# Kernel optimization log

Hardware: AMD Instinct MI355X
Metric: run time of the kernel (lower is better)

Reference implementation:

```python
import jax, jax.numpy as jnp
import numpy as np

# ragged segment lengths (sum = 100000), 16 graphs of varying size
LENGTHS = np.array([3000, 5000, 7000, 2000, 9000, 4000, 6000, 8000,
                    1000, 10000, 5500, 6500, 7500, 4500, 9500, 11500], dtype=np.int64)

B, N, C_IN, K_DIM, Q_DIM, C_OUT = 4, 100000, 256, 64, 64, 128


def setup_inputs() -> dict:
    key = jax.random.key(0)
    ks = jax.random.split(key, 6)
    features = jax.random.normal(ks[0], (B, N, C_IN), dtype=jnp.float32)
    # linear-layer params (stored as [in, out]; torch Linear computes x @ W.T + b)
    Wk = jax.random.normal(ks[1], (C_IN, K_DIM), dtype=jnp.float32) / np.sqrt(C_IN)
    bk = jnp.zeros((K_DIM,), dtype=jnp.float32)
    Wq = jax.random.normal(ks[2], (C_IN, Q_DIM), dtype=jnp.float32) / np.sqrt(C_IN)
    bq = jnp.zeros((Q_DIM,), dtype=jnp.float32)
    Wv = jax.random.normal(ks[3], (C_IN, C_OUT), dtype=jnp.float32) / np.sqrt(C_IN)
    return {"features": features, "lengths": LENGTHS,
            "Wk": Wk, "bk": bk, "Wq": Wq, "bq": bq, "Wv": Wv}


def reference(features, lengths, Wk, bk, Wq, bq, Wv):
    # projections + (elu + 1) feature map for keys/queries
    k = jax.nn.elu(features @ Wk + bk) + 1.0   # [B, N, K]
    q = jax.nn.elu(features @ Wq + bq) + 1.0   # [B, N, Q]
    v = features @ Wv                           # [B, N, O]
    # static ragged offsets (lengths is a concrete numpy array)
    offs = np.concatenate([[0], np.cumsum(np.asarray(lengths))]).astype(np.int64)
    outs = []
    for i in range(len(offs) - 1):  # loop over fixed small set of graphs
        s, e = int(offs[i]), int(offs[i + 1])
        ktv = jnp.einsum('bnk,bno->bko', k[:, s:e], v[:, s:e])   # per-segment K^T V
        outs.append(jnp.einsum('bnq,bqo->bno', q[:, s:e], ktv))  # Q (K^T V)
    return jnp.concatenate(outs, axis=1)  # [B, N, O]
```

## Files before the change

### kernel.cpp

```cpp
#include <hip/hip_runtime.h>

#define B_ 4
#define N_ 100000

typedef unsigned short u16;
typedef unsigned int u32;
typedef __attribute__((ext_vector_type(8))) __bf16 bf16x8;
typedef __attribute__((ext_vector_type(4))) float floatx4;

__device__ const int d_OFFS[17]  = {0,3000,8000,15000,17000,26000,30000,36000,44000,45000,55000,60500,67000,74500,79000,88500,100000};
__device__ const int d_CH128[17] = {0,24,64,119,135,206,238,285,348,356,435,478,529,588,624,699,789};

__device__ __forceinline__ u16 f2bf(float f) {
    union { float f; unsigned u; } x; x.f = f;
    unsigned r = x.u + 0x7fffu + ((x.u >> 16) & 1u);
    return (u16)(r >> 16);
}

union U4 { u32 u[4]; bf16x8 v; uint4 q; };

__global__ void prep_kernel(const float* __restrict__ Wk, const float* __restrict__ bk,
                            const float* __restrict__ Wq, const float* __restrict__ bq,
                            const float* __restrict__ Wv,
                            u16* __restrict__ Bt, float* __restrict__ bias,
                            float* __restrict__ ktvF) {
    int idx = blockIdx.x * 256 + threadIdx.x;
    int n = idx >> 8, kk = idx & 255;
    float w;
    if (n < 64)        w = Wk[kk*64 + n];
    else if (n < 128)  w = Wq[kk*64 + (n-64)];
    else               w = Wv[kk*128 + (n-128)];
    Bt[n*256 + kk] = f2bf(w);
    if (blockIdx.x == 0) {
        int c = threadIdx.x;
        bias[c] = (c < 64) ? bk[c] : (c < 128 ? bq[c-64] : 0.f);
    }
    float4 z = {0.f, 0.f, 0.f, 0.f};
    float4* zd = (float4*)ktvF + (long)idx * 2;
    zd[0] = z; zd[1] = z;
}

__global__ __launch_bounds__(512, 4) void proj_kernel(const float* __restrict__ feat,
        const u16* __restrict__ Bt, const float* __restrict__ bias,
        u16* __restrict__ qws, float* __restrict__ ktvF) {
    __shared__ __attribute__((aligned(16))) char smem[50176];
    u16 (*ldsA)[40] = (u16(*)[40])smem;
    u16 (*ldsB)[40] = (u16(*)[40])(smem + 10240);
    u16 (*Kl)[66]   = (u16(*)[66])smem;
    u16 (*Vl)[130]  = (u16(*)[130])(smem + 16896);

    const int t = threadIdx.x, lane = t & 63, wave = t >> 6;
    const int wrow = wave & 1, wcol = wave >> 1;
    const long row0 = (long)blockIdx.x * 128;

    floatx4 acc[4][4];
    #pragma unroll
    for (int i = 0; i < 4; ++i)
        #pragma unroll
        for (int j = 0; j < 4; ++j) acc[i][j] = (floatx4)(0.f);

    const int asr = t >> 2, ask = (t & 3) * 8;
    const int bsr = t >> 1, bsk = (t & 1) * 16;

    float4 pf0, pf1; uint4 pb0, pb1;
    {
        const float* src = feat + (row0 + asr) * 256 + ask;
        pf0 = *(const float4*)(src); pf1 = *(const float4*)(src + 4);
        const u16* bsrc = Bt + bsr*256 + bsk;
        pb0 = *(const uint4*)bsrc; pb1 = *(const uint4*)(bsrc + 8);
    }

    for (int kc = 0; kc < 8; ++kc) {
        __syncthreads();
        {
            u16 tmp[8] __attribute__((aligned(16)));
            tmp[0]=f2bf(pf0.x); tmp[1]=f2bf(pf0.y); tmp[2]=f2bf(pf0.z); tmp[3]=f2bf(pf0.w);
            tmp[4]=f2bf(pf1.x); tmp[5]=f2bf(pf1.y); tmp[6]=f2bf(pf1.z); tmp[7]=f2bf(pf1.w);
            *(uint4*)&ldsA[asr][ask] = *(const uint4*)tmp;
            *(uint4*)&ldsB[bsr][bsk]   = pb0;
            *(uint4*)&ldsB[bsr][bsk+8] = pb1;
        }
        __syncthreads();
        if (kc < 7) {
            const float* src = feat + (row0 + asr) * 256 + (kc+1)*32 + ask;
            pf0 = *(const float4*)(src); pf1 = *(const float4*)(src + 4);
            const u16* bsrc = Bt + bsr*256 + (kc+1)*32 + bsk;
            pb0 = *(const uint4*)bsrc; pb1 = *(const uint4*)(bsrc + 8);
        }
        bf16x8 af[4];
        #pragma unroll
        for (int mt = 0; mt < 4; ++mt)
            af[mt] = *(const bf16x8*)&ldsA[wrow*64 + mt*16 + (lane & 15)][(lane >> 4) * 8];
        #pragma unroll
        for (int nt = 0; nt < 4; ++nt) {
            bf16x8 bfv = *(const bf16x8*)&ldsB[wcol*64 + nt*16 + (lane & 15)][(lane >> 4) * 8];
            #pragma unroll
            for (int mt = 0; mt < 4; ++mt)
                acc[mt][nt] = __builtin_amdgcn_mfma_f32_16x16x32_bf16(af[mt], bfv, acc[mt][nt], 0, 0, 0);
        }
    }

    __syncthreads();
    #pragma unroll
    for (int nt = 0; nt < 4; ++nt) {
        int col = wcol*64 + nt*16 + (lane & 15);
        float bc = (col < 128) ? bias[col] : 0.f;
        #pragma unroll
        for (int mt = 0; mt < 4; ++mt) {
            #pragma unroll
            for (int reg = 0; reg < 4; ++reg) {
                int r = wrow*64 + mt*16 + (lane >> 4)*4 + reg;
                float val = acc[mt][nt][reg] + bc;
                if (col < 64) {
                    val = (val > 0.f) ? (val + 1.f) : __expf(val);
                    Kl[r][col] = f2bf(val);
                } else if (col < 128) {
                    val = (val > 0.f) ? (val + 1.f) : __expf(val);
                    qws[(row0 + r)*64 + (col-64)] = f2bf(val);
                } else {
                    Vl[r][col-128] = f2bf(val);
                }
            }
        }
    }

    const long rlast = row0 + 127;
    const int b0 = (int)(row0 / N_), n0r = (int)(row0 % N_);
    const int b1 = (int)(rlast / N_), n1r = (int)(rlast % N_);
    int s0 = 0, s1 = 0;
    #pragma unroll
    for (int s = 0; s < 16; ++s) {
        if (n0r >= d_OFFS[s+1]) s0 = s + 1;
        if (n1r >= d_OFFS[s+1]) s1 = s + 1;
    }
    const int id0 = s0*4 + b0, id1 = s1*4 + b1;
    const long split = (long)b1 * N_ + d_OFFS[s1];
    const int npass = (id0 == id1) ? 1 : 2;

    __syncthreads();

    const int mt2 = wave >> 1;
    const int oq  = wave & 1;
    const int kdr = mt2*16 + (lane & 15);
    for (int pass = 0; pass < npass; ++pass) {
        bf16x8 afr[4];
        #pragma unroll
        for (int ks = 0; ks < 4; ++ks) {
            u16 tmp[8] __attribute__((aligned(16)));
            #pragma unroll
            for (int j = 0; j < 8; ++j) {
                int nn = ks*32 + (lane >> 4)*8 + j;
                u16 hv = Kl[nn][kdr];
                if (npass == 2 && (((row0 + nn) >= split) != (pass == 1))) hv = 0;
                tmp[j] = hv;
            }
            afr[ks] = *(const bf16x8*)tmp;
        }
        floatx4 kacc[4];
        #pragma unroll
        for (int i = 0; i < 4; ++i) kacc[i] = (floatx4)(0.f);
        #pragma unroll
        for (int ot = 0; ot < 4; ++ot) {
            int o = (oq*4 + ot)*16 + (lane & 15);
            #pragma unroll
            for (int ks = 0; ks < 4; ++ks) {
                u16 tmp[8] __attribute__((aligned(16)));
                #pragma unroll
                for (int j = 0; j < 8; ++j)
                    tmp[j] = Vl[ks*32 + (lane >> 4)*8 + j][o];
                kacc[ot] = __builtin_amdgcn_mfma_f32_16x16x32_bf16(afr[ks], *(const bf16x8*)tmp, kacc[ot], 0, 0, 0);
            }
        }
        float* dst = ktvF + (long)(pass ? id1 : id0) * 8192;
        #pragma unroll
        for (int ot = 0; ot < 4; ++ot) {
            int o = (oq*4 + ot)*16 + (lane & 15);
            #pragma unroll
            for (int reg = 0; reg < 4; ++reg) {
                int kd = mt2*16 + (lane >> 4)*4 + reg;
                atomicAdd(dst + kd*128 + o, kacc[ot][reg]);
            }
        }
    }
}

__global__ __launch_bounds__(256) void out_kernel(const u16* __restrict__ qws,
                                                  const float* __restrict__ ktvF,
                                                  float* __restrict__ out) {
    __shared__ u16 ldsA[128][72];
    __shared__ u16 ldsB[128][72];
    const int t = threadIdx.x, lane = t & 63, wave = t >> 6;
    const int wrow = wave & 1, wcol = wave >> 1;
    const int b = blockIdx.y, cid = blockIdx.x;
    int seg = 0;
    #pragma unroll
    for (int s = 0; s < 16; ++s) if (cid >= d_CH128[s+1]) seg = s + 1;
    const int n0   = d_OFFS[seg] + (cid - d_CH128[seg]) * 128;
    const int nend = d_OFFS[seg+1];
    const int sb = seg*4 + b;

    floatx4 acc[4][4];
    #pragma unroll
    for (int i = 0; i < 4; ++i)
        #pragma unroll
        for (int j = 0; j < 4; ++j) acc[i][j] = (floatx4)(0.f);

    const int sr = t >> 1, kh = (t & 1) * 32;
    {
        int n = n0 + sr;
        if (n < nend) {
            const u16* src = qws + ((long)b * N_ + n)*64 + kh;
            #pragma unroll
            for (int i = 0; i < 4; ++i)
                *(uint4*)&ldsA[sr][kh + i*8] = *(const uint4*)(src + i*8);
        } else {
            uint4 z = {0,0,0,0};
            #pragma unroll
            for (int i = 0; i < 4; ++i) *(uint4*)&ldsA[sr][kh + i*8] = z;
        }
        const float* bsrc = ktvF + (long)sb * 8192 + sr;
        #pragma unroll
        for (int i = 0; i < 4; ++i) {
            u16 tmp[8] __attribute__((aligned(16)));
            #pragma unroll
            for (int j = 0; j < 8; ++j)
                tmp[j] = f2bf(bsrc[(long)(kh + i*8 + j) * 128]);
            *(uint4*)&ldsB[sr][kh + i*8] = *(const uint4*)tmp;
        }
    }
    __syncthreads();
    #pragma unroll
    for (int kc = 0; kc < 2; ++kc) {
        bf16x8 af[4];
        #pragma unroll
        for (int mt = 0; mt < 4; ++mt)
            af[mt] = *(const bf16x8*)&ldsA[wrow*64 + mt*16 + (lane & 15)][kc*32 + (lane >> 4)*8];
        #pragma unroll
        for (int nt = 0; nt < 4; ++nt) {
            bf16x8 bfv = *(const bf16x8*)&ldsB[wcol*64 + nt*16 + (lane & 15)][kc*32 + (lane >> 4)*8];
            #pragma unroll
            for (int mt = 0; mt < 4; ++mt)
                acc[mt][nt] = __builtin_amdgcn_mfma_f32_16x16x32_bf16(af[mt], bfv, acc[mt][nt], 0, 0, 0);
        }
    }
    #pragma unroll
    for (int nt = 0; nt < 4; ++nt) {
        int col = wcol*64 + nt*16 + (lane & 15);
        #pragma unroll
        for (int mt = 0; mt < 4; ++mt)
            #pragma unroll
            for (int reg = 0; reg < 4; ++reg) {
                int n = n0 + wrow*64 + mt*16 + (lane >> 4)*4 + reg;
                if (n < nend)
                    out[((long)b * N_ + n)*128 + col] = acc[mt][nt][reg];
            }
    }
}

extern "C" void kernel_launch(void* const* d_in, const int* in_sizes, int n_in,
                              void* d_out, int out_size, void* d_ws, size_t ws_size,
                              hipStream_t stream) {
    (void)in_sizes; (void)n_in; (void)out_size; (void)ws_size;
    const float* feat = (const float*)d_in[0];
    const float* Wk = (const float*)d_in[2];
    const float* bk = (const float*)d_in[3];
    const float* Wq = (const float*)d_in[4];
    const float* bq = (const float*)d_in[5];
    const float* Wv = (const float*)d_in[6];
    float* out = (float*)d_out;

    char* ws = (char*)d_ws;
    u16*   qws  = (u16*)  (ws);
    u16*   Bt   = (u16*)  (ws + 51200000);
    float* bias = (float*)(ws + 51331072);
    float* ktvF = (float*)(ws + 51332096);

    prep_kernel<<<256, 256, 0, stream>>>(Wk, bk, Wq, bq, Wv, Bt, bias, ktvF);
    proj_kernel<<<3125, 512, 0, stream>>>(feat, Bt, bias, qws, ktvF);
    out_kernel<<<dim3(789, 4), 256, 0, stream>>>(qws, ktvF, out);
}
```

Baseline: 744.0 us.

## Load GEMM fragments directly from global memory and transpose K/V staging in LDS

The projection GEMM main loop no longer stages feature and weight tiles through LDS behind two barriers per k-step. Each wave now loads its MFMA A/B fragments straight from global memory into registers. K and V are stored transposed in LDS so the K^T V MFMA operands become contiguous vector reads instead of strided scalar gathers. The output kernel also reads Q fragments directly from global memory rather than through LDS. This removes barriers and LDS traffic, but adds redundant global loads, since fragments are now fetched per wave, and uncoalesced row-strided access patterns.

```diff
diff --git a/kernel.cpp b/kernel.cpp
--- a/kernel.cpp
+++ b/kernel.cpp
@@ -43,13 +43,11 @@
 __global__ __launch_bounds__(512, 4) void proj_kernel(const float* __restrict__ feat,
         const u16* __restrict__ Bt, const float* __restrict__ bias,
         u16* __restrict__ qws, float* __restrict__ ktvF) {
-    __shared__ __attribute__((aligned(16))) char smem[50176];
-    u16 (*ldsA)[40] = (u16(*)[40])smem;
-    u16 (*ldsB)[40] = (u16(*)[40])(smem + 10240);
-    u16 (*Kl)[66]   = (u16(*)[66])smem;
-    u16 (*Vl)[130]  = (u16(*)[130])(smem + 16896);
+    __shared__ u16 Kt[64][136];
+    __shared__ u16 Vt[128][136];
 
     const int t = threadIdx.x, lane = t & 63, wave = t >> 6;
+    const int q = lane >> 4, r15 = lane & 15;
     const int wrow = wave & 1, wcol = wave >> 1;
     const long row0 = (long)blockIdx.x * 128;
 
@@ -59,125 +57,133 @@
         #pragma unroll
         for (int j = 0; j < 4; ++j) acc[i][j] = (floatx4)(0.f);
 
-    const int asr = t >> 2, ask = (t & 3) * 8;
-    const int bsr = t >> 1, bsk = (t & 1) * 16;
-
-    float4 pf0, pf1; uint4 pb0, pb1;
-    {
-        const float* src = feat + (row0 + asr) * 256 + ask;
-        pf0 = *(const float4*)(src); pf1 = *(const float4*)(src + 4);
-        const u16* bsrc = Bt + bsr*256 + bsk;
-        pb0 = *(const uint4*)bsrc; pb1 = *(const uint4*)(bsrc + 8);
-    }
-
+    const float* ap0 = feat + (row0 + wrow*64 +  0 + r15) * 256 + q*8;
+    const float* ap1 = feat + (row0 + wrow*64 + 16 + r15) * 256 + q*8;
+    const float* ap2 = feat + (row0 + wrow*64 + 32 + r15) * 256 + q*8;
+    const float* ap3 = feat + (row0 + wrow*64 + 48 + r15) * 256 + q*8;
+    const u16* bp0 = Bt + (wcol*64 +  0 + r15) * 256 + q*8;
+    const u16* bp1 = Bt + (wcol*64 + 16 + r15) * 256 + q*8;
+    const u16* bp2 = Bt + (wcol*64 + 32 + r15) * 256 + q*8;
+    const u16* bp3 = Bt + (wcol*64 + 48 + r15) * 256 + q*8;
+
+    #pragma unroll 2
     for (int kc = 0; kc < 8; ++kc) {
-        __syncthreads();
+        const int ko = kc * 32;
+        float4 a00 = *(const float4*)(ap0 + ko), a01 = *(const float4*)(ap0 + ko + 4);
+        float4 a10 = *(const float4*)(ap1 + ko), a11 = *(const float4*)(ap1 + ko + 4);
+        float4 a20 = *(const float4*)(ap2 + ko), a21 = *(const float4*)(ap2 + ko + 4);
+        float4 a30 = *(const float4*)(ap3 + ko), a31 = *(const float4*)(ap3 + ko + 4);
+        U4 b0, b1, b2, b3;
+        b0.q = *(const uint4*)(bp0 + ko);
+        b1.q = *(const uint4*)(bp1 + ko);
+        b2.q = *(const uint4*)(bp2 + ko);
+        b3.q = *(const uint4*)(bp3 + ko);
+
+        bf16x8 af[4];
         {
             u16 tmp[8] __attribute__((aligned(16)));
-            tmp[0]=f2bf(pf0.x); tmp[1]=f2bf(pf0.y); tmp[2]=f2bf(pf0.z); tmp[3]=f2bf(pf0.w);
-            tmp[4]=f2bf(pf1.x); tmp[5]=f2bf(pf1.y); tmp[6]=f2bf(pf1.z); tmp[7]=f2bf(pf1.w);
-            *(uint4*)&ldsA[asr][ask] = *(const uint4*)tmp;
-            *(uint4*)&ldsB[bsr][bsk]   = pb0;
-            *(uint4*)&ldsB[bsr][bsk+8] = pb1;
-        }
-        __syncthreads();
-        if (kc < 7) {
-            const float* src = feat + (row0 + asr) * 256 + (kc+1)*32 + ask;
-            pf0 = *(const float4*)(src); pf1 = *(const float4*)(src + 4);
-            const u16* bsrc = Bt + bsr*256 + (kc+1)*32 + bsk;
-            pb0 = *(const uint4*)bsrc; pb1 = *(const uint4*)(bsrc + 8);
-        }
-        bf16x8 af[4];
-        #pragma unroll
-        for (int mt = 0; mt < 4; ++mt)
-            af[mt] = *(const bf16x8*)&ldsA[wrow*64 + mt*16 + (lane & 15)][(lane >> 4) * 8];
-        #pragma unroll
-        for (int nt = 0; nt < 4; ++nt) {
-            bf16x8 bfv = *(const bf16x8*)&ldsB[wcol*64 + nt*16 + (lane & 15)][(lane >> 4) * 8];
-            #pragma unroll
-            for (int mt = 0; mt < 4; ++mt)
-                acc[mt][nt] = __builtin_amdgcn_mfma_f32_16x16x32_bf16(af[mt], bfv, acc[mt][nt], 0, 0, 0);
-        }
-    }
-
-    __syncthreads();
+            tmp[0]=f2bf(a00.x); tmp[1]=f2bf(a00.y); tmp[2]=f2bf(a00.z); tmp[3]=f2bf(a00.w);
+            tmp[4]=f2bf(a01.x); tmp[5]=f2bf(a01.y); tmp[6]=f2bf(a01.z); tmp[7]=f2bf(a01.w);
+            af[0] = *(const bf16x8*)tmp;
+            tmp[0]=f2bf(a10.x); tmp[1]=f2bf(a10.y); tmp[2]=f2bf(a10.z); tmp[3]=f2bf(a10.w);
+            tmp[4]=f2bf(a11.x); tmp[5]=f2bf(a11.y); tmp[6]=f2bf(a11.z); tmp[7]=f2bf(a11.w);
+            af[1] = *(const bf16x8*)tmp;
+            tmp[0]=f2bf(a20.x); tmp[1]=f2bf(a20.y); tmp[2]=f2bf(a20.z); tmp[3]=f2bf(a20.w);
+            tmp[4]=f2bf(a21.x); tmp[5]=f2bf(a21.y); tmp[6]=f2bf(a21.z); tmp[7]=f2bf(a21.w);
+            af[2] = *(const bf16x8*)tmp;
+            tmp[0]=f2bf(a30.x); tmp[1]=f2bf(a30.y); tmp[2]=f2bf(a30.z); tmp[3]=f2bf(a30.w);
+            tmp[4]=f2bf(a31.x); tmp[5]=f2bf(a31.y); tmp[6]=f2bf(a31.z); tmp[7]=f2bf(a31.w);
+            af[3] = *(const bf16x8*)tmp;
+        }
+        #pragma unroll
+        for (int mt = 0; mt < 4; ++mt) {
+            acc[mt][0] = __builtin_amdgcn_mfma_f32_16x16x32_bf16(af[mt], b0.v, acc[mt][0], 0, 0, 0);
+            acc[mt][1] = __builtin_amdgcn_mfma_f32_16x16x32_bf16(af[mt], b1.v, acc[mt][1], 0, 0, 0);
+            acc[mt][2] = __builtin_amdgcn_mfma_f32_16x16x32_bf16(af[mt], b2.v, acc[mt][2], 0, 0, 0);
+            acc[mt][3] = __builtin_amdgcn_mfma_f32_16x16x32_bf16(af[mt], b3.v, acc[mt][3], 0, 0, 0);
+        }
+    }
+
     #pragma unroll
     for (int nt = 0; nt < 4; ++nt) {
-        int col = wcol*64 + nt*16 + (lane & 15);
+        int col = wcol*64 + nt*16 + r15;
         float bc = (col < 128) ? bias[col] : 0.f;
         #pragma unroll
         for (int mt = 0; mt < 4; ++mt) {
             #pragma unroll
             for (int reg = 0; reg < 4; ++reg) {
-                int r = wrow*64 + mt*16 + (lane >> 4)*4 + reg;
+                int r = wrow*64 + mt*16 + q*4 + reg;
                 float val = acc[mt][nt][reg] + bc;
                 if (col < 64) {
                     val = (val > 0.f) ? (val + 1.f) : __expf(val);
-                    Kl[r][col] = f2bf(val);
+                    Kt[col][r] = f2bf(val);
                 } else if (col < 128) {
                     val = (val > 0.f) ? (val + 1.f) : __expf(val);
                     qws[(row0 + r)*64 + (col-64)] = f2bf(val);
                 } else {
-                    Vl[r][col-128] = f2bf(val);
+                    Vt[col-128][r] = f2bf(val);
                 }
             }
         }
     }
 
     const long rlast = row0 + 127;
-    const int b0 = (int)(row0 / N_), n0r = (int)(row0 % N_);
-    const int b1 = (int)(rlast / N_), n1r = (int)(rlast % N_);
+    const int b0i = (int)(row0 / N_), n0r = (int)(row0 % N_);
+    const int b1i = (int)(rlast / N_), n1r = (int)(rlast % N_);
     int s0 = 0, s1 = 0;
     #pragma unroll
     for (int s = 0; s < 16; ++s) {
         if (n0r >= d_OFFS[s+1]) s0 = s + 1;
         if (n1r >= d_OFFS[s+1]) s1 = s + 1;
     }
-    const int id0 = s0*4 + b0, id1 = s1*4 + b1;
-    const long split = (long)b1 * N_ + d_OFFS[s1];
+    const int id0 = s0*4 + b0i, id1 = s1*4 + b1i;
+    const long split = (long)b1i * N_ + d_OFFS[s1];
     const int npass = (id0 == id1) ? 1 : 2;
 
     __syncthreads();
 
     const int mt2 = wave >> 1;
     const int oq  = wave & 1;
-    const int kdr = mt2*16 + (lane & 15);
+    const int kdr = mt2*16 + r15;
     for (int pass = 0; pass < npass; ++pass) {
         bf16x8 afr[4];
-        #pragma unroll
-        for (int ks = 0; ks < 4; ++ks) {
-            u16 tmp[8] __attribute__((aligned(16)));
-            #pragma unroll
-            for (int j = 0; j < 8; ++j) {
-                int nn = ks*32 + (lane >> 4)*8 + j;
-                u16 hv = Kl[nn][kdr];
-                if (npass == 2 && (((row0 + nn) >= split) != (pass == 1))) hv = 0;
-                tmp[j] = hv;
-            }
-            afr[ks] = *(const bf16x8*)tmp;
-        }
-        floatx4 kacc[4];
-        #pragma unroll
-        for (int i = 0; i < 4; ++i) kacc[i] = (floatx4)(0.f);
-        #pragma unroll
-        for (int ot = 0; ot < 4; ++ot) {
-            int o = (oq*4 + ot)*16 + (lane & 15);
+        if (npass == 1) {
+            #pragma unroll
+            for (int ks = 0; ks < 4; ++ks)
+                afr[ks] = *(const bf16x8*)&Kt[kdr][ks*32 + q*8];
+        } else {
             #pragma unroll
             for (int ks = 0; ks < 4; ++ks) {
                 u16 tmp[8] __attribute__((aligned(16)));
                 #pragma unroll
-                for (int j = 0; j < 8; ++j)
-                    tmp[j] = Vl[ks*32 + (lane >> 4)*8 + j][o];
-                kacc[ot] = __builtin_amdgcn_mfma_f32_16x16x32_bf16(afr[ks], *(const bf16x8*)tmp, kacc[ot], 0, 0, 0);
+                for (int j = 0; j < 8; ++j) {
+                    int nn = ks*32 + q*8 + j;
+                    u16 hv = Kt[kdr][nn];
+                    if (((row0 + nn) >= split) != (pass == 1)) hv = 0;
+                    tmp[j] = hv;
+                }
+                afr[ks] = *(const bf16x8*)tmp;
+            }
+        }
+        floatx4 kacc[4];
+        #pragma unroll
+        for (int i = 0; i < 4; ++i) kacc[i] = (floatx4)(0.f);
+        #pragma unroll
+        for (int ot = 0; ot < 4; ++ot) {
+            int o = (oq*4 + ot)*16 + r15;
+            #pragma unroll
+            for (int ks = 0; ks < 4; ++ks) {
+                bf16x8 bfr = *(const bf16x8*)&Vt[o][ks*32 + q*8];
+                kacc[ot] = __builtin_amdgcn_mfma_f32_16x16x32_bf16(afr[ks], bfr, kacc[ot], 0, 0, 0);
             }
         }
         float* dst = ktvF + (long)(pass ? id1 : id0) * 8192;
         #pragma unroll
         for (int ot = 0; ot < 4; ++ot) {
-            int o = (oq*4 + ot)*16 + (lane & 15);
+            int o = (oq*4 + ot)*16 + r15;
             #pragma unroll
             for (int reg = 0; reg < 4; ++reg) {
-                int kd = mt2*16 + (lane >> 4)*4 + reg;
+                int kd = mt2*16 + q*4 + reg;
                 atomicAdd(dst + kd*128 + o, kacc[ot][reg]);
             }
         }
@@ -187,9 +193,9 @@
 __global__ __launch_bounds__(256) void out_kernel(const u16* __restrict__ qws,
                                                   const float* __restrict__ ktvF,
                                                   float* __restrict__ out) {
-    __shared__ u16 ldsA[128][72];
     __shared__ u16 ldsB[128][72];
     const int t = threadIdx.x, lane = t & 63, wave = t >> 6;
+    const int q = lane >> 4, r15 = lane & 15;
     const int wrow = wave & 1, wcol = wave >> 1;
     const int b = blockIdx.y, cid = blockIdx.x;
     int seg = 0;
@@ -199,25 +205,8 @@
     const int nend = d_OFFS[seg+1];
     const int sb = seg*4 + b;
 
-    floatx4 acc[4][4];
-    #pragma unroll
-    for (int i = 0; i < 4; ++i)
-        #pragma unroll
-        for (int j = 0; j < 4; ++j) acc[i][j] = (floatx4)(0.f);
-
-    const int sr = t >> 1, kh = (t & 1) * 32;
     {
-        int n = n0 + sr;
-        if (n < nend) {
-            const u16* src = qws + ((long)b * N_ + n)*64 + kh;
-            #pragma unroll
-            for (int i = 0; i < 4; ++i)
-                *(uint4*)&ldsA[sr][kh + i*8] = *(const uint4*)(src + i*8);
-        } else {
-            uint4 z = {0,0,0,0};
-            #pragma unroll
-            for (int i = 0; i < 4; ++i) *(uint4*)&ldsA[sr][kh + i*8] = z;
-        }
+        const int sr = t >> 1, kh = (t & 1) * 32;
         const float* bsrc = ktvF + (long)sb * 8192 + sr;
         #pragma unroll
         for (int i = 0; i < 4; ++i) {
@@ -228,16 +217,29 @@
             *(uint4*)&ldsB[sr][kh + i*8] = *(const uint4*)tmp;
         }
     }
+
+    floatx4 acc[4][4];
+    #pragma unroll
+    for (int i = 0; i < 4; ++i)
+        #pragma unroll
+        for (int j = 0; j < 4; ++j) acc[i][j] = (floatx4)(0.f);
+
     __syncthreads();
+
+    U4 zu; zu.u[0] = zu.u[1] = zu.u[2] = zu.u[3] = 0;
     #pragma unroll
     for (int kc = 0; kc < 2; ++kc) {
         bf16x8 af[4];
         #pragma unroll
-        for (int mt = 0; mt < 4; ++mt)
-            af[mt] = *(const bf16x8*)&ldsA[wrow*64 + mt*16 + (lane & 15)][kc*32 + (lane >> 4)*8];
+        for (int mt = 0; mt < 4; ++mt) {
+            int n = n0 + wrow*64 + mt*16 + r15;
+            af[mt] = (n < nend)
+                ? *(const bf16x8*)(qws + ((long)b * N_ + n)*64 + kc*32 + q*8)
+                : zu.v;
+        }
         #pragma unroll
         for (int nt = 0; nt < 4; ++nt) {
-            bf16x8 bfv = *(const bf16x8*)&ldsB[wcol*64 + nt*16 + (lane & 15)][kc*32 + (lane >> 4)*8];
+            bf16x8 bfv = *(const bf16x8*)&ldsB[wcol*64 + nt*16 + r15][kc*32 + q*8];
             #pragma unroll
             for (int mt = 0; mt < 4; ++mt)
                 acc[mt][nt] = __builtin_amdgcn_mfma_f32_16x16x32_bf16(af[mt], bfv, acc[mt][nt], 0, 0, 0);
@@ -245,12 +247,12 @@
     }
     #pragma unroll
     for (int nt = 0; nt < 4; ++nt) {
-        int col = wcol*64 + nt*16 + (lane & 15);
+        int col = wcol*64 + nt*16 + r15;
         #pragma unroll
         for (int mt = 0; mt < 4; ++mt)
             #pragma unroll
             for (int reg = 0; reg < 4; ++reg) {
-                int n = n0 + wrow*64 + mt*16 + (lane >> 4)*4 + reg;
+                int n = n0 + wrow*64 + mt*16 + q*4 + reg;
                 if (n < nend)
                     out[((long)b * N_ + n)*128 + col] = acc[mt][nt][reg];
             }
```

Measured after the change: 883.2 us. 1.19x slower.
